# Kernel optimization log

Measured on AMD Instinct MI355X. Metric: run time of the kernel, lower is better.

Reference implementation:

```python
import jax, jax.numpy as jnp
import numpy as np

VARIANCES = (0.1, 0.2)
THRESHOLD = 0.35
NEG_POS = 7
NUM_CLASSES = 3
B, P, G = 64, 32768, 64


def point_form(boxes):
    # (cx,cy,w,h) -> (x1,y1,x2,y2)
    return jnp.concatenate([boxes[:, :2] - boxes[:, 2:] / 2,
                            boxes[:, :2] + boxes[:, 2:] / 2], axis=1)


def jaccard(a, b):
    # a: [G,4], b: [P,4], both point-form -> IoU [G,P]
    lt = jnp.maximum(a[:, None, :2], b[None, :, :2])
    rb = jnp.minimum(a[:, None, 2:], b[None, :, 2:])
    wh = jnp.clip(rb - lt, 0.0)
    inter = wh[..., 0] * wh[..., 1]
    area_a = (a[:, 2] - a[:, 0]) * (a[:, 3] - a[:, 1])
    area_b = (b[:, 2] - b[:, 0]) * (b[:, 3] - b[:, 1])
    return inter / (area_a[:, None] + area_b[None, :] - inter)


def encode(matched, priors):
    # matched point-form [P,4], priors center-form [P,4]
    g_cxcy = ((matched[:, :2] + matched[:, 2:]) / 2 - priors[:, :2]) / (VARIANCES[0] * priors[:, 2:])
    g_wh = jnp.log((matched[:, 2:] - matched[:, :2]) / priors[:, 2:]) / VARIANCES[1]
    return jnp.concatenate([g_cxcy, g_wh], axis=1)


def encode_landm(matched, priors):
    # matched [P,10] -> [P,5,2] offsets
    m = matched.reshape(-1, 5, 2)
    g = (m - priors[:, None, :2]) / (VARIANCES[0] * priors[:, None, 2:])
    return g.reshape(-1, 10)


def match_one(truths, labels, landms, priors, priors_pt):
    overlaps = jaccard(truths, priors_pt)                     # [G,P]
    best_prior_overlap = overlaps.max(axis=1)                 # [G]
    best_prior_idx = overlaps.argmax(axis=1)                  # [G]
    valid_gt = best_prior_overlap >= 0.2                      # filter hard gt
    any_valid = valid_gt.any()
    best_truth_overlap = overlaps.max(axis=0)                 # [P]
    best_truth_idx = overlaps.argmax(axis=0)                  # [P]
    # force-match: each valid gt claims its best prior (overlap set to 2 > threshold)
    best_truth_overlap = best_truth_overlap.at[best_prior_idx].max(jnp.where(valid_gt, 2.0, -1.0))
    best_truth_idx = best_truth_idx.at[best_prior_idx].set(jnp.arange(truths.shape[0]))
    matches = truths[best_truth_idx]                          # [P,4]
    conf = labels[best_truth_idx].astype(jnp.int32)           # [P]
    conf = jnp.where(best_truth_overlap < THRESHOLD, 0, conf)
    loc = encode(matches, priors)
    landm = encode_landm(landms[best_truth_idx], priors)
    # early-return branch of match(): no valid gt -> loc_t = 0, conf_t = 0
    loc = jnp.where(any_valid, loc, 0.0)
    conf = jnp.where(any_valid, conf, 0)
    return loc, conf, landm


def smooth_l1(d):
    ad = jnp.abs(d)
    return jnp.where(ad < 1.0, 0.5 * d * d, ad - 0.5)


def setup_inputs() -> dict:
    key = jax.random.key(0)
    k1, k2, k3, k4, k5, k6, k7, k8 = jax.random.split(key, 8)
    loc_data = jax.random.normal(k1, (B, P, 4), dtype=jnp.float32)
    conf_data = jax.random.normal(k2, (B, P, NUM_CLASSES), dtype=jnp.float32)
    landm_data = jax.random.normal(k3, (B, P, 10), dtype=jnp.float32)
    # priors: center-form, in (0,1)
    cxcy = jax.random.uniform(k4, (P, 2), dtype=jnp.float32)
    pwh = jax.random.uniform(k5, (P, 2), dtype=jnp.float32) * 0.28 + 0.02
    priors = jnp.concatenate([cxcy, pwh], axis=1)
    # targets: [B,G,15] = 4 box (point-form) + 10 landm + 1 label in {1,2}
    x1y1 = jax.random.uniform(k6, (B, G, 2), dtype=jnp.float32) * 0.8
    twh = jax.random.uniform(k7, (B, G, 2), dtype=jnp.float32) * 0.18 + 0.02
    lm = jax.random.uniform(k8, (B, G, 10), dtype=jnp.float32)
    lbl = jax.random.randint(jax.random.fold_in(key, 9), (B, G, 1), 1, 3).astype(jnp.float32)
    targets = jnp.concatenate([x1y1, x1y1 + twh, lm, lbl], axis=2)
    return {"loc_data": loc_data, "conf_data": conf_data, "landm_data": landm_data,
            "priors": priors, "targets": targets}


def reference(loc_data, conf_data, landm_data, priors, targets):
    num, num_priors = loc_data.shape[0], priors.shape[0]
    priors_pt = point_form(priors)
    truths, landms, labels = targets[:, :, :4], targets[:, :, 4:14], targets[:, :, 14]
    loc_t, conf_t, landm_t = jax.vmap(match_one, in_axes=(0, 0, 0, None, None))(
        truths, labels, landms, priors, priors_pt)
    loc_t = jax.lax.stop_gradient(loc_t)      # torch builds targets from .data
    landm_t = jax.lax.stop_gradient(landm_t)
    f32 = jnp.float32
    # ---- landmark loss (face: all 10 coords; mask: first 4 coords only) ----
    N1 = jnp.maximum((conf_t > 0).sum().astype(f32), 1.0)
    face = (conf_t == 1)[..., None]
    maskc = (conf_t == 2)[..., None]
    el = smooth_l1(landm_data - landm_t)                      # [B,P,10]
    loss_landm = (el * face).sum() + (el[..., :4] * maskc).sum()
    # ---- localization loss over all positives ----
    pos = conf_t != 0
    loss_l = (smooth_l1(loc_data - loc_t) * pos[..., None]).sum()
    # ---- hard negative mining + confidence loss ----
    conf_t2 = jnp.where(conf_t < 0, 1, conf_t)                # no-landmark faces -> class 1
    lse = jax.nn.logsumexp(conf_data, axis=-1)                # [B,P]
    gathered = jnp.take_along_axis(conf_data, conf_t2[..., None], axis=-1)[..., 0]
    loss_c = jnp.where(pos, 0.0, lse - gathered)              # [B,P]
    loss_idx = jnp.argsort(-loss_c, axis=1)                   # sort descending
    idx_rank = jnp.argsort(loss_idx, axis=1)                  # rank of each prior
    num_pos = pos.sum(axis=1, keepdims=True)
    num_neg = jnp.minimum(NEG_POS * num_pos, num_priors - 1)
    neg = idx_rank < num_neg
    sel = pos | neg
    loss_c_final = jnp.where(sel, lse - gathered, 0.0).sum()
    N = jnp.maximum(num_pos.sum().astype(f32), 1.0)
    return (loss_l / N, loss_c_final / N, loss_landm / N1)
```

## Files before the change

### kernel.cpp

```cpp
#include <hip/hip_runtime.h>

#define B 64
#define P 32768
#define G 64


__device__ __forceinline__ float sl1(float d) {
    float ad = fabsf(d);
    return (ad < 1.0f) ? 0.5f * d * d : (ad - 0.5f);
}

__global__ void k0_init(const float* __restrict__ priors, const float* __restrict__ targets,
                        float* __restrict__ priors_pre, float* __restrict__ truth_pre,
                        unsigned long long* __restrict__ bp_packed,
                        int* __restrict__ num_pos, int* __restrict__ any_valid,
                        double* __restrict__ acc) {
    int i = blockIdx.x * 256 + threadIdx.x;
    if (i < P) {
        float4 pr = ((const float4*)priors)[i];
        float px1 = pr.x - pr.z * 0.5f, py1 = pr.y - pr.w * 0.5f;
        float px2 = pr.x + pr.z * 0.5f, py2 = pr.y + pr.w * 0.5f;
        float area = (px2 - px1) * (py2 - py1);
        float* o = priors_pre + (size_t)i * 8;
        o[0] = px1; o[1] = py1; o[2] = px2; o[3] = py2; o[4] = area; o[5] = 0.f; o[6] = 0.f; o[7] = 0.f;
    }
    if (i < B * G) {
        const float* t = targets + (size_t)i * 15;
        float x1 = t[0], y1 = t[1], x2 = t[2], y2 = t[3];
        float* o = truth_pre + (size_t)i * 8;
        o[0] = x1; o[1] = y1; o[2] = x2; o[3] = y2;
        o[4] = (x2 - x1) * (y2 - y1); o[5] = t[14]; o[6] = 0.f; o[7] = 0.f;
        bp_packed[i] = 0ull;
    }
    if (i < B) { num_pos[i] = 0; any_valid[i] = 0; }
    if (i < 8) acc[i] = 0.0;
}

__launch_bounds__(256, 4)
__global__ void k1_match(const float* __restrict__ priors_pre, const float* __restrict__ truth_pre,
                         float* __restrict__ bto, int* __restrict__ bti,
                         unsigned long long* __restrict__ bp_packed) {
    __shared__ float ious[32 * 257];
    __shared__ unsigned long long part[256];
    int b = blockIdx.y, tid = threadIdx.x;
    int p = blockIdx.x * 256 + tid;

    const float4 q = *(const float4*)(priors_pre + (size_t)p * 8);
    float pa = priors_pre[(size_t)p * 8 + 4];
    float px1 = q.x, py1 = q.y, px2 = q.z, py2 = q.w;

    float bestv = 0.f;
    int bestg = 0;

    for (int half = 0; half < 2; ++half) {
        for (int j = 0; j < 32; ++j) {
            int g = half * 32 + j;
            const float* t = truth_pre + ((size_t)b * G + g) * 8;
            float lx = fmaxf(px1, t[0]);
            float ly = fmaxf(py1, t[1]);
            float rx = fminf(px2, t[2]);
            float ry = fminf(py2, t[3]);
            float w = fmaxf(rx - lx, 0.f), h = fmaxf(ry - ly, 0.f);
            float inter = w * h;
            float denom = pa + t[4] - inter;
            float iou = inter * __builtin_amdgcn_rcpf(denom);
            ious[j * 257 + tid] = iou;
            if (iou > bestv) { bestv = iou; bestg = g; }
        }
        __syncthreads();
        int gr = tid & 31, c = tid >> 5;
        unsigned long long best = 0ull;
        int pbase = blockIdx.x * 256 + c * 32;
        for (int j = 0; j < 32; ++j) {
            float v = ious[gr * 257 + c * 32 + j];
            unsigned long long pk =
                ((unsigned long long)__float_as_uint(v) << 32) | (unsigned int)(~(pbase + j));
            if (pk > best) best = pk;
        }
        part[tid] = best;
        __syncthreads();
        if (tid < 32) {
            unsigned long long m = part[tid];
#pragma unroll
            for (int cc = 1; cc < 8; ++cc) {
                unsigned long long o = part[tid + cc * 32];
                if (o > m) m = o;
            }
            atomicMax(&bp_packed[b * G + half * 32 + tid], m);
        }
        __syncthreads();
    }
    bto[(size_t)b * P + p] = bestv;
    bti[(size_t)b * P + p] = bestg;
}

__global__ void k2_force(const unsigned long long* __restrict__ bp_packed,
                         float* __restrict__ bto, int* __restrict__ bti,
                         int* __restrict__ any_valid) {
    int b = blockIdx.x, g = threadIdx.x;
    unsigned long long pk = bp_packed[b * G + g];
    float bpo = __uint_as_float((unsigned int)(pk >> 32));
    unsigned int bpi = ~((unsigned int)pk);
    bool valid = bpo >= 0.2f;
    unsigned long long ball = __ballot(valid);
    if (g == 0) any_valid[b] = (ball != 0ull) ? 1 : 0;
    if (valid) bto[(size_t)b * P + bpi] = 2.0f;
    atomicMax(&bti[(size_t)b * P + bpi], 256 + g);
}

__launch_bounds__(256, 4)
__global__ void k3_loss(const float* __restrict__ loc_data, const float* __restrict__ conf_data,
                        const float* __restrict__ landm_data, const float* __restrict__ priors,
                        const float* __restrict__ targets,
                        const float* __restrict__ bto, const int* __restrict__ bti,
                        const int* __restrict__ any_valid,
                        float* __restrict__ c_neg, int* __restrict__ num_pos,
                        float4* __restrict__ part3) {
    __shared__ float st[G * 15];
    __shared__ float rbuf[12];
    __shared__ int ribuf[4];
    int b = blockIdx.y, tid = threadIdx.x;
    int p = blockIdx.x * 256 + tid;
    for (int i = tid; i < G * 15; i += 256) st[i] = targets[(size_t)b * G * 15 + i];
    __syncthreads();

    size_t idx = (size_t)b * P + p;
    int v = bti[idx];
    int g = (v >= 256) ? (v - 256) : v;
    float ov = bto[idx];
    int conf = 0;
    if (any_valid[b] != 0 && ov >= 0.35f) conf = (int)st[g * 15 + 14];

    const float* cd = conf_data + idx * 3;
    float c0 = cd[0], c1 = cd[1], c2 = cd[2];
    float m = fmaxf(c0, fmaxf(c1, c2));
    float lse = m + __logf(__expf(c0 - m) + __expf(c1 - m) + __expf(c2 - m));
    float gath = (conf == 0) ? c0 : ((conf == 1) ? c1 : c2);
    float lc = lse - gath;

    float cn = 0.f, lloss = 0.f, lmloss = 0.f, plse = 0.f;
    int np = 0;
    if (conf != 0) { np = 1; plse = lc; }
    else cn = fmaxf(lc, 0.f);
    c_neg[idx] = cn;

    if (conf != 0) {
        float4 pr = ((const float4*)priors)[p];
        const float* t = st + g * 15;
        float t0 = t[0], t1 = t[1], t2 = t[2], t3 = t[3];
        float gcx = ((t0 + t2) * 0.5f - pr.x) / (0.1f * pr.z);
        float gcy = ((t1 + t3) * 0.5f - pr.y) / (0.1f * pr.w);
        float gw = __logf((t2 - t0) / pr.z) / 0.2f;
        float gh = __logf((t3 - t1) / pr.w) / 0.2f;
        float4 ld = ((const float4*)loc_data)[idx];
        lloss = sl1(ld.x - gcx) + sl1(ld.y - gcy) + sl1(ld.z - gw) + sl1(ld.w - gh);

        int dims = (conf == 1) ? 10 : 4;
        const float* lmd = landm_data + idx * 10;
        for (int d = 0; d < dims; ++d) {
            float pc = (d & 1) ? pr.y : pr.x;
            float ps = (d & 1) ? pr.w : pr.z;
            float gv = (t[4 + d] - pc) / (0.1f * ps);
            lmloss += sl1(lmd[d] - gv);
        }
    }

    for (int off = 32; off > 0; off >>= 1) {
        lloss  += __shfl_down(lloss, off);
        plse   += __shfl_down(plse, off);
        lmloss += __shfl_down(lmloss, off);
        np     += __shfl_down(np, off);
    }
    int wave = tid >> 6, lane = tid & 63;
    if (lane == 0) { rbuf[wave] = lloss; rbuf[4 + wave] = plse; rbuf[8 + wave] = lmloss; ribuf[wave] = np; }
    __syncthreads();
    if (tid == 0) {
        float a = rbuf[0] + rbuf[1] + rbuf[2] + rbuf[3];
        float bb = rbuf[4] + rbuf[5] + rbuf[6] + rbuf[7];
        float cc = rbuf[8] + rbuf[9] + rbuf[10] + rbuf[11];
        int n = ribuf[0] + ribuf[1] + ribuf[2] + ribuf[3];
        part3[b * gridDim.x + blockIdx.x] = make_float4(a, bb, cc, (float)n);
        if (n) atomicAdd(&num_pos[b], n);
    }
}

__launch_bounds__(1024, 1)
__global__ void k4_mine(const float* __restrict__ c_neg, const int* __restrict__ num_pos,
                        double* __restrict__ acc) {
    __shared__ unsigned int hist[16][256];
    __shared__ unsigned int chist[256];
    __shared__ unsigned int sh_prefix, sh_rem;
    __shared__ double sd[16];
    __shared__ unsigned int sc[16];
    int b = blockIdx.x, tid = threadIdx.x;
    int wv = tid >> 6, lane = tid & 63;
    int npb = num_pos[b];
    long long k = 7LL * npb;
    if (k > P - 1) k = P - 1;
    if (k <= 0) return;
    const float* cb = c_neg + (size_t)b * P;

    unsigned int prefix = 0, remaining = (unsigned int)k;
    for (int byte = 3; byte >= 0; --byte) {
        for (int i = tid; i < 16 * 256; i += 1024) ((unsigned int*)hist)[i] = 0;
        __syncthreads();
        int shift = byte * 8;
        if (byte == 3) {
            for (int i = tid; i < P; i += 1024) {
                unsigned int u = __float_as_uint(cb[i]);
                unsigned int bin = u >> 24;
                unsigned long long todo = __ballot(true);
                while (todo) {
                    int src = (int)(__ffsll((unsigned long long)todo) - 1);
                    unsigned int lbin = (unsigned int)__shfl((int)bin, src);
                    unsigned long long mm = __ballot(bin == lbin);
                    if (lane == src) atomicAdd(&hist[wv][lbin], (unsigned int)__popcll(mm));
                    todo &= ~mm;
                }
            }
        } else {
            unsigned int himask = 0xFFFFFFFFu << (shift + 8);
            for (int i = tid; i < P; i += 1024) {
                unsigned int u = __float_as_uint(cb[i]);
                if ((u & himask) == (prefix & himask))
                    atomicAdd(&hist[wv][(u >> shift) & 255u], 1u);
            }
        }
        __syncthreads();
        if (tid < 256) {
            unsigned int s = 0;
#pragma unroll
            for (int w = 0; w < 16; ++w) s += hist[w][tid];
            chist[tid] = s;
        }
        __syncthreads();
        if (wv == 0) {
            int b0 = 255 - 4 * lane;
            unsigned int c0 = chist[b0], c1 = chist[b0 - 1], c2 = chist[b0 - 2], c3 = chist[b0 - 3];
            unsigned int csum = c0 + c1 + c2 + c3;
            unsigned int scan = csum;
            for (int off = 1; off < 64; off <<= 1) {
                unsigned int o = (unsigned int)__shfl_up((int)scan, off);
                if (lane >= off) scan += o;
            }
            unsigned int excl = scan - csum;
            if (scan >= remaining && excl < remaining) {
                int selbin; unsigned int below;
                if (excl + c0 >= remaining)                 { selbin = b0;     below = excl; }
                else if (excl + c0 + c1 >= remaining)       { selbin = b0 - 1; below = excl + c0; }
                else if (excl + c0 + c1 + c2 >= remaining)  { selbin = b0 - 2; below = excl + c0 + c1; }
                else                                        { selbin = b0 - 3; below = excl + c0 + c1 + c2; }
                sh_prefix = prefix | ((unsigned int)selbin << shift);
                sh_rem = remaining - below;
            }
        }
        __syncthreads();
        prefix = sh_prefix; remaining = sh_rem;
        __syncthreads();
    }
    float t = __uint_as_float(prefix);

    double s = 0.0; unsigned int cgt = 0;
    for (int i = tid; i < P; i += 1024) {
        float v = cb[i];
        if (v > t) { s += (double)v; cgt++; }
    }
    for (int off = 32; off > 0; off >>= 1) {
        s += __shfl_down(s, off);
        cgt += __shfl_down(cgt, off);
    }
    if (lane == 0) { sd[wv] = s; sc[wv] = cgt; }
    __syncthreads();
    if (tid == 0) {
        double tot = 0.0; unsigned int cg = 0;
#pragma unroll
        for (int w = 0; w < 16; ++w) { tot += sd[w]; cg += sc[w]; }
        tot += (double)(k - (long long)cg) * (double)t;
        atomicAdd(&acc[1], tot);
    }
}

__global__ void k5_final(const float4* __restrict__ part3, const int* __restrict__ num_pos,
                         const double* __restrict__ acc, float* __restrict__ out,
                         int nparts) {
    __shared__ double sb[3][4];
    int tid = threadIdx.x;
    double sl = 0.0, scn = 0.0, sm = 0.0;
    for (int i = tid; i < nparts; i += 256) {
        float4 v = part3[i];
        sl += (double)v.x; scn += (double)v.y; sm += (double)v.z;
    }
    for (int off = 32; off > 0; off >>= 1) {
        sl += __shfl_down(sl, off);
        scn += __shfl_down(scn, off);
        sm += __shfl_down(sm, off);
    }
    int wave = tid >> 6, lane = tid & 63;
    if (lane == 0) { sb[0][wave] = sl; sb[1][wave] = scn; sb[2][wave] = sm; }
    __syncthreads();
    if (tid == 0) {
        double L = sb[0][0] + sb[0][1] + sb[0][2] + sb[0][3];
        double C = sb[1][0] + sb[1][1] + sb[1][2] + sb[1][3] + acc[1];
        double M = sb[2][0] + sb[2][1] + sb[2][2] + sb[2][3];
        int n = 0;
        for (int i = 0; i < B; ++i) n += num_pos[i];
        double N = (double)(n < 1 ? 1 : n);
        out[0] = (float)(L / N);
        out[1] = (float)(C / N);
        out[2] = (float)(M / N);
    }
}

extern "C" void kernel_launch(void* const* d_in, const int* in_sizes, int n_in,
                              void* d_out, int out_size, void* d_ws, size_t ws_size,
                              hipStream_t stream) {
    const float* loc     = (const float*)d_in[0];
    const float* confd   = (const float*)d_in[1];
    const float* landm   = (const float*)d_in[2];
    const float* priors  = (const float*)d_in[3];
    const float* targets = (const float*)d_in[4];
    float* out = (float*)d_out;

    char* ws = (char*)d_ws;
    double* acc                  = (double*)(ws + 0);
    int* num_pos                 = (int*)(ws + 256);
    int* any_valid               = (int*)(ws + 512);
    unsigned long long* bp       = (unsigned long long*)(ws + 1024);
    float* truth_pre             = (float*)(ws + 33792);
    float* priors_pre            = (float*)(ws + 164864);
    float4* part3                = (float4*)(ws + 164864);
    float* bto                   = (float*)(ws + 1213440);
    int* bti                     = (int*)(ws + 9602048);
    float* c_neg                 = (float*)(ws + 17990656);

    k0_init<<<dim3(P / 256), dim3(256), 0, stream>>>(priors, targets, priors_pre, truth_pre,
                                                     bp, num_pos, any_valid, acc);
    k1_match<<<dim3(P / 256, B), dim3(256), 0, stream>>>(priors_pre, truth_pre, bto, bti, bp);
    k2_force<<<dim3(B), dim3(64), 0, stream>>>(bp, bto, bti, any_valid);
    k3_loss<<<dim3(P / 256, B), dim3(256), 0, stream>>>(loc, confd, landm, priors, targets,
                                                        bto, bti, any_valid, c_neg, num_pos, part3);
    k4_mine<<<dim3(B), dim3(1024), 0, stream>>>(c_neg, num_pos, acc);
    k5_final<<<1, 256, 0, stream>>>(part3, num_pos, acc, out, (P / 256) * B);
}
```

Measured before the change: 364.6 us.

## Use wave shuffle reductions for per-gt best prior in match kernel

The match kernel drops the shared-memory IoU tile and its two-pass block reduction. For each ground truth it now takes a wave-wide max through shuffle-xor, finds the first lane with ballot, and folds the packed (value, index) into a small shared array with atomics, followed by one global atomicMax per gt. Prior point-form conversion moves into the match kernel, so the init kernel shrinks and the priors_pre buffer goes away. Occupancy launch bounds are raised. The cost is six shuffles per gt per wave instead of one shared-memory pass, and ties between equal IoUs are now broken by lowest index within each wave.

```diff
diff --git a/kernel.cpp b/kernel.cpp
--- a/kernel.cpp
+++ b/kernel.cpp
@@ -10,20 +10,11 @@
     return (ad < 1.0f) ? 0.5f * d * d : (ad - 0.5f);
 }
 
-__global__ void k0_init(const float* __restrict__ priors, const float* __restrict__ targets,
-                        float* __restrict__ priors_pre, float* __restrict__ truth_pre,
+__global__ void k0_init(const float* __restrict__ targets, float* __restrict__ truth_pre,
                         unsigned long long* __restrict__ bp_packed,
                         int* __restrict__ num_pos, int* __restrict__ any_valid,
                         double* __restrict__ acc) {
     int i = blockIdx.x * 256 + threadIdx.x;
-    if (i < P) {
-        float4 pr = ((const float4*)priors)[i];
-        float px1 = pr.x - pr.z * 0.5f, py1 = pr.y - pr.w * 0.5f;
-        float px2 = pr.x + pr.z * 0.5f, py2 = pr.y + pr.w * 0.5f;
-        float area = (px2 - px1) * (py2 - py1);
-        float* o = priors_pre + (size_t)i * 8;
-        o[0] = px1; o[1] = py1; o[2] = px2; o[3] = py2; o[4] = area; o[5] = 0.f; o[6] = 0.f; o[7] = 0.f;
-    }
     if (i < B * G) {
         const float* t = targets + (size_t)i * 15;
         float x1 = t[0], y1 = t[1], x2 = t[2], y2 = t[3];
@@ -36,60 +27,53 @@
     if (i < 8) acc[i] = 0.0;
 }
 
-__launch_bounds__(256, 4)
-__global__ void k1_match(const float* __restrict__ priors_pre, const float* __restrict__ truth_pre,
+__launch_bounds__(256, 8)
+__global__ void k1_match(const float* __restrict__ priors, const float* __restrict__ truth_pre,
                          float* __restrict__ bto, int* __restrict__ bti,
                          unsigned long long* __restrict__ bp_packed) {
-    __shared__ float ious[32 * 257];
-    __shared__ unsigned long long part[256];
+    __shared__ unsigned long long lbp[G];
     int b = blockIdx.y, tid = threadIdx.x;
+    int lane = tid & 63;
     int p = blockIdx.x * 256 + tid;
-
-    const float4 q = *(const float4*)(priors_pre + (size_t)p * 8);
-    float pa = priors_pre[(size_t)p * 8 + 4];
-    float px1 = q.x, py1 = q.y, px2 = q.z, py2 = q.w;
+    int pbase_wave = blockIdx.x * 256 + (tid & ~63);
+
+    float4 pr = ((const float4*)priors)[p];
+    float px1 = pr.x - pr.z * 0.5f, py1 = pr.y - pr.w * 0.5f;
+    float px2 = pr.x + pr.z * 0.5f, py2 = pr.y + pr.w * 0.5f;
+    float pa = (px2 - px1) * (py2 - py1);
+
+    if (tid < G) lbp[tid] = 0ull;
+    __syncthreads();
 
     float bestv = 0.f;
     int bestg = 0;
-
-    for (int half = 0; half < 2; ++half) {
-        for (int j = 0; j < 32; ++j) {
-            int g = half * 32 + j;
-            const float* t = truth_pre + ((size_t)b * G + g) * 8;
-            float lx = fmaxf(px1, t[0]);
-            float ly = fmaxf(py1, t[1]);
-            float rx = fminf(px2, t[2]);
-            float ry = fminf(py2, t[3]);
-            float w = fmaxf(rx - lx, 0.f), h = fmaxf(ry - ly, 0.f);
-            float inter = w * h;
-            float denom = pa + t[4] - inter;
-            float iou = inter * __builtin_amdgcn_rcpf(denom);
-            ious[j * 257 + tid] = iou;
-            if (iou > bestv) { bestv = iou; bestg = g; }
-        }
-        __syncthreads();
-        int gr = tid & 31, c = tid >> 5;
-        unsigned long long best = 0ull;
-        int pbase = blockIdx.x * 256 + c * 32;
-        for (int j = 0; j < 32; ++j) {
-            float v = ious[gr * 257 + c * 32 + j];
-            unsigned long long pk =
-                ((unsigned long long)__float_as_uint(v) << 32) | (unsigned int)(~(pbase + j));
-            if (pk > best) best = pk;
-        }
-        part[tid] = best;
-        __syncthreads();
-        if (tid < 32) {
-            unsigned long long m = part[tid];
+    const float* tb = truth_pre + (size_t)b * G * 8;
+
+#pragma unroll 4
+    for (int g = 0; g < G; ++g) {
+        const float* t = tb + g * 8;
+        float lx = fmaxf(px1, t[0]);
+        float ly = fmaxf(py1, t[1]);
+        float rx = fminf(px2, t[2]);
+        float ry = fminf(py2, t[3]);
+        float w = fmaxf(rx - lx, 0.f), h = fmaxf(ry - ly, 0.f);
+        float inter = w * h;
+        float denom = (pa + t[4]) - inter;
+        float iou = inter * __builtin_amdgcn_rcpf(denom);
+        bool better = iou > bestv;
+        bestv = better ? iou : bestv;
+        bestg = better ? g : bestg;
+        float m = iou;
 #pragma unroll
-            for (int cc = 1; cc < 8; ++cc) {
-                unsigned long long o = part[tid + cc * 32];
-                if (o > m) m = o;
-            }
-            atomicMax(&bp_packed[b * G + half * 32 + tid], m);
-        }
-        __syncthreads();
-    }
+        for (int off = 1; off < 64; off <<= 1) m = fmaxf(m, __shfl_xor(m, off));
+        unsigned long long msk = __ballot(iou == m);
+        int src = __ffsll((long long)msk) - 1;
+        unsigned long long pk = ((unsigned long long)__float_as_uint(m) << 32)
+                              | (unsigned int)~(unsigned int)(pbase_wave + src);
+        if (lane == 0) atomicMax(&lbp[g], pk);
+    }
+    __syncthreads();
+    if (tid < G) atomicMax(&bp_packed[b * G + tid], lbp[tid]);
     bto[(size_t)b * P + p] = bestv;
     bti[(size_t)b * P + p] = bestg;
 }
@@ -211,7 +195,7 @@
                 unsigned int bin = u >> 24;
                 unsigned long long todo = __ballot(true);
                 while (todo) {
-                    int src = (int)(__ffsll((unsigned long long)todo) - 1);
+                    int src = (int)(__ffsll((long long)todo) - 1);
                     unsigned int lbin = (unsigned int)__shfl((int)bin, src);
                     unsigned long long mm = __ballot(bin == lbin);
                     if (lane == src) atomicAdd(&hist[wv][lbin], (unsigned int)__popcll(mm));
@@ -327,15 +311,14 @@
     int* any_valid               = (int*)(ws + 512);
     unsigned long long* bp       = (unsigned long long*)(ws + 1024);
     float* truth_pre             = (float*)(ws + 33792);
-    float* priors_pre            = (float*)(ws + 164864);
     float4* part3                = (float4*)(ws + 164864);
     float* bto                   = (float*)(ws + 1213440);
     int* bti                     = (int*)(ws + 9602048);
     float* c_neg                 = (float*)(ws + 17990656);
 
-    k0_init<<<dim3(P / 256), dim3(256), 0, stream>>>(priors, targets, priors_pre, truth_pre,
-                                                     bp, num_pos, any_valid, acc);
-    k1_match<<<dim3(P / 256, B), dim3(256), 0, stream>>>(priors_pre, truth_pre, bto, bti, bp);
+    k0_init<<<dim3((B * G) / 256), dim3(256), 0, stream>>>(targets, truth_pre,
+                                                           bp, num_pos, any_valid, acc);
+    k1_match<<<dim3(P / 256, B), dim3(256), 0, stream>>>(priors, truth_pre, bto, bti, bp);
     k2_force<<<dim3(B), dim3(64), 0, stream>>>(bp, bto, bti, any_valid);
     k3_loss<<<dim3(P / 256, B), dim3(256), 0, stream>>>(loc, confd, landm, priors, targets,
                                                         bto, bti, any_valid, c_neg, num_pos, part3);
```

New measurement: 451.2 us. 1.24x slower.
